# Optimization experiments

Measured on AMD Instinct MI355X. Metric: run time of the kernel, lower is better.

Reference implementation:

```python
import jax, jax.numpy as jnp
import numpy as np

B, C, T, H, W = 2, 512, 4, 32, 32
NH = 8          # num_heads
GROUPS = 32     # GroupNorm groups
EPS = 1e-5      # GroupNorm eps (torch default)


def setup_inputs() -> dict:
    key = jax.random.key(0)
    k0, k1, k2 = jax.random.split(key, 3)
    s = 0.02
    return {
        "x": jax.random.normal(k0, (B, C, T, H, W), jnp.float32),
        "gn_w": jnp.ones((C,), jnp.float32),
        "gn_b": jnp.zeros((C,), jnp.float32),
        "qkv_w": jax.random.normal(k1, (3 * C, C), jnp.float32) * s,
        "qkv_b": jnp.zeros((3 * C,), jnp.float32),
        "out_w": jax.random.normal(k2, (C, C), jnp.float32) * s,
        "out_b": jnp.zeros((C,), jnp.float32),
    }


def reference(x, gn_w, gn_b, qkv_w, qkv_b, out_w, out_b):
    Bb, Cc, Tt, Hh, Ww = x.shape
    N = Tt * Hh * Ww
    hd = Cc // NH

    # GroupNorm(32, C): normalize over (C//G, T, H, W) per group, biased var
    xg = x.reshape(Bb, GROUPS, -1)
    mean = jnp.mean(xg, axis=-1, keepdims=True)
    var = jnp.var(xg, axis=-1, keepdims=True)
    h = ((xg - mean) * jax.lax.rsqrt(var + EPS)).reshape(Bb, Cc, N)
    h = h * gn_w[None, :, None] + gn_b[None, :, None]

    # 1x1 Conv3d qkv == per-token linear over channels
    qkv = jnp.einsum('oc,bcn->bon', qkv_w, h) + qkv_b[None, :, None]
    qkv = qkv.reshape(Bb, 3, NH, hd, N).transpose(1, 0, 2, 4, 3)  # [3,B,nh,N,hd]
    q, k, v = qkv[0], qkv[1], qkv[2]

    scale = 1.0 / np.sqrt(hd).astype(np.float32)
    attn = jax.nn.softmax(jnp.einsum('bhnd,bhmd->bhnm', q, k) * scale, axis=-1)
    o = jnp.einsum('bhnm,bhmd->bhnd', attn, v)  # [B,nh,N,hd]

    # Faithful to original: h.permute(1,2,0,3).reshape(B,C,T,H,W)
    o = o.transpose(1, 2, 0, 3).reshape(Bb, Cc, N)
    o = jnp.einsum('oc,bcn->bon', out_w, o) + out_b[None, :, None]
    return x + o.reshape(Bb, Cc, Tt, Hh, Ww)
```

## Files before the change

### kernel.cpp

```cpp
#include <hip/hip_runtime.h>
#include <stdint.h>

#define B_    2
#define C_    512
#define NH_   8
#define HD_   64
#define N_    4096
#define G_    32
#define K_    512
#define EPS_  1e-5f
#define QSCALE_ 0.18033688011112042f

typedef __bf16 bf16;
typedef __attribute__((ext_vector_type(8))) __bf16 bf16x8;
typedef __attribute__((ext_vector_type(4))) float f32x4;

__global__ __launch_bounds__(256) void prep_k(const float* __restrict__ qkv_w,
                                              const float* __restrict__ out_w,
                                              const float* __restrict__ x,
                                              bf16* __restrict__ qkvwb,
                                              bf16* __restrict__ outwb,
                                              float* __restrict__ part) {
  const int blk = blockIdx.x;
  const int t = threadIdx.x;
  if (blk < 1024) {
    const int i = blk * 256 + t;
    const int n0 = (3 * C_ * C_) / 4;
    const float* s = (i < n0) ? qkv_w : out_w;
    bf16* d = (i < n0) ? qkvwb : outwb;
    const int k = (i < n0) ? i : i - n0;
    f32x4 v = *reinterpret_cast<const f32x4*>(s + (size_t)k * 4);
    bf16 o[4] = {(bf16)v[0], (bf16)v[1], (bf16)v[2], (bf16)v[3]};
    *reinterpret_cast<uint64_t*>(d + (size_t)k * 4) = *reinterpret_cast<uint64_t*>(o);
  } else {
    const int bb = blk - 1024;
    const float* p = x + (size_t)bb * 16384;
    float s1 = 0.f, s2 = 0.f;
    for (int i = 0; i < 16; ++i) {
      f32x4 v = *reinterpret_cast<const f32x4*>(p + (size_t)(i * 256 + t) * 4);
#pragma unroll
      for (int j = 0; j < 4; ++j) { float f = v[j]; s1 += f; s2 += f * f; }
    }
#pragma unroll
    for (int o = 32; o > 0; o >>= 1) { s1 += __shfl_down(s1, o); s2 += __shfl_down(s2, o); }
    __shared__ float a1[4], a2[4];
    if ((t & 63) == 0) { a1[t >> 6] = s1; a2[t >> 6] = s2; }
    __syncthreads();
    if (t == 0) {
      part[bb * 2]     = a1[0] + a1[1] + a1[2] + a1[3];
      part[bb * 2 + 1] = a2[0] + a2[1] + a2[2] + a2[3];
    }
  }
}

__global__ __launch_bounds__(256) void gn_apply_k(const float* __restrict__ x,
                                                  const float* __restrict__ part,
                                                  const float* __restrict__ gw,
                                                  const float* __restrict__ gb,
                                                  bf16* __restrict__ hT) {
  __shared__ float tile[64][65];
  const int n0 = blockIdx.x * 64, c0 = blockIdx.y * 64, b = blockIdx.z;
  const int t = threadIdx.x;
  {
    const int cc = t >> 2;
    const int nn = (t & 3) * 16;
    const int c = c0 + cc;
    const int bg = b * G_ + (c >> 4);
    float s1 = 0.f, s2 = 0.f;
#pragma unroll
    for (int q = 0; q < 4; ++q) {
      s1 += part[(bg * 4 + q) * 2];
      s2 += part[(bg * 4 + q) * 2 + 1];
    }
    const float mean = s1 * (1.f / 65536.f);
    const float var  = s2 * (1.f / 65536.f) - mean * mean;
    const float rstd = rsqrtf(var + EPS_);
    const float sw = gw[c] * rstd;
    const float sb = gb[c] - mean * sw;
    const float* xp = x + ((size_t)(b * C_ + c)) * N_ + n0 + nn;
#pragma unroll
    for (int q = 0; q < 4; ++q) {
      f32x4 v = *reinterpret_cast<const f32x4*>(xp + q * 4);
#pragma unroll
      for (int j = 0; j < 4; ++j) tile[cc][nn + q * 4 + j] = v[j] * sw + sb;
    }
  }
  __syncthreads();
  {
    const int rn = t >> 2;
    const int ch = (t & 3) * 16;
    bf16* hp = hT + ((size_t)b * N_ + n0 + rn) * C_ + c0 + ch;
    bf16x8 o0, o1;
#pragma unroll
    for (int j = 0; j < 8; ++j) {
      o0[j] = (bf16)tile[ch + j][rn];
      o1[j] = (bf16)tile[ch + 8 + j][rn];
    }
    *reinterpret_cast<bf16x8*>(hp)     = o0;
    *reinterpret_cast<bf16x8*>(hp + 8) = o1;
  }
}

template <int EPI>
__global__ __launch_bounds__(256) void gemm_bt_k(const bf16* __restrict__ A,
                                                 const bf16* __restrict__ BT,
                                                 const float* __restrict__ bias,
                                                 bf16* __restrict__ out0,
                                                 bf16* __restrict__ out1,
                                                 bf16* __restrict__ out2,
                                                 float* __restrict__ outf,
                                                 const float* __restrict__ xres) {
  __shared__ __align__(16) bf16 As[128][72];
  __shared__ __align__(16) bf16 Bs[128][72];
  const int t = threadIdx.x;
  const int w = t >> 6, lane = t & 63;
  const int quad = lane >> 4, l15 = lane & 15;
  const int m0 = blockIdx.y * 128, n0 = blockIdx.x * 128, b = blockIdx.z;
  const bf16* Ab = A + (size_t)m0 * K_;
  const bf16* Bb = BT + ((size_t)b * N_ + n0) * K_;
  const int srow = t >> 1;
  const int sk = (t & 1) * 32;

  f32x4 acc[4][4] = {};

  for (int kc = 0; kc < K_ / 64; ++kc) {
    __syncthreads();
    {
      const bf16* ag = Ab + (size_t)srow * K_ + kc * 64 + sk;
      const bf16* bg = Bb + (size_t)srow * K_ + kc * 64 + sk;
#pragma unroll
      for (int c = 0; c < 4; ++c) {
        *reinterpret_cast<bf16x8*>(&As[srow][sk + c * 8]) = *reinterpret_cast<const bf16x8*>(ag + c * 8);
        *reinterpret_cast<bf16x8*>(&Bs[srow][sk + c * 8]) = *reinterpret_cast<const bf16x8*>(bg + c * 8);
      }
    }
    __syncthreads();
    bf16x8 af[4][2], bfv[4][2];
#pragma unroll
    for (int i = 0; i < 4; ++i) {
      af[i][0] = *reinterpret_cast<const bf16x8*>(&As[(w >> 1) * 64 + i * 16 + l15][quad * 8]);
      af[i][1] = *reinterpret_cast<const bf16x8*>(&As[(w >> 1) * 64 + i * 16 + l15][quad * 8 + 32]);
    }
#pragma unroll
    for (int j = 0; j < 4; ++j) {
      bfv[j][0] = *reinterpret_cast<const bf16x8*>(&Bs[(w & 1) * 64 + j * 16 + l15][quad * 8]);
      bfv[j][1] = *reinterpret_cast<const bf16x8*>(&Bs[(w & 1) * 64 + j * 16 + l15][quad * 8 + 32]);
    }
#pragma unroll
    for (int i = 0; i < 4; ++i)
#pragma unroll
      for (int j = 0; j < 4; ++j) {
        acc[i][j] = __builtin_amdgcn_mfma_f32_16x16x32_bf16(af[i][0], bfv[j][0], acc[i][j], 0, 0, 0);
        acc[i][j] = __builtin_amdgcn_mfma_f32_16x16x32_bf16(af[i][1], bfv[j][1], acc[i][j], 0, 0, 0);
      }
  }

  const int rowbase = m0 + (w >> 1) * 64;
  const int colbase = n0 + (w & 1) * 64;
  if (EPI == 0) {
    const int which = m0 >> 9;
    if (which < 2) {
      bf16* dst = (which == 0) ? out0 : out1;
      const float sc = (which == 0) ? (float)QSCALE_ : 1.0f;
#pragma unroll
      for (int i = 0; i < 4; ++i) {
        const int mbase = rowbase + i * 16 + quad * 4;
        const int head = (mbase >> 6) & 7, d0 = mbase & 63;
        float bi[4];
#pragma unroll
        for (int r = 0; r < 4; ++r) bi[r] = bias[mbase + r];
#pragma unroll
        for (int j = 0; j < 4; ++j) {
          const int n = colbase + j * 16 + l15;
          union { bf16 h[4]; uint64_t u; } pk;
#pragma unroll
          for (int r = 0; r < 4; ++r) pk.h[r] = (bf16)((acc[i][j][r] + bi[r]) * sc);
          *reinterpret_cast<uint64_t*>(dst + ((size_t)(b * NH_ + head) * N_ + n) * HD_ + d0) = pk.u;
        }
      }
    } else {
#pragma unroll
      for (int i = 0; i < 4; ++i) {
        const int mbase = rowbase + i * 16 + quad * 4;
        const int head = (mbase >> 6) & 7;
#pragma unroll
        for (int r = 0; r < 4; ++r) {
          const int d = (mbase + r) & 63;
          const float bi = bias[mbase + r];
#pragma unroll
          for (int j = 0; j < 4; ++j) {
            const int n = colbase + j * 16 + l15;
            out2[((size_t)(b * NH_ + head) * HD_ + d) * N_ + n] = (bf16)(acc[i][j][r] + bi);
          }
        }
      }
    }
  } else {
#pragma unroll
    for (int i = 0; i < 4; ++i) {
#pragma unroll
      for (int r = 0; r < 4; ++r) {
        const int m = rowbase + i * 16 + quad * 4 + r;
        const float bi = bias[m];
#pragma unroll
        for (int j = 0; j < 4; ++j) {
          const int n = colbase + j * 16 + l15;
          const size_t idx = ((size_t)(b * C_ + m)) * N_ + n;
          outf[idx] = acc[i][j][r] + bi + xres[idx];
        }
      }
    }
  }
}

__global__ __launch_bounds__(256, 3) void attn_k(const bf16* __restrict__ qb,
                                                 const bf16* __restrict__ kb,
                                                 const bf16* __restrict__ vb,
                                                 bf16* __restrict__ oT) {
  __shared__ __align__(16) char smem[46080];
  bf16* Ps = (bf16*)(smem + 36864);
  bf16* Ot = (bf16*)smem;

  const int t = threadIdx.x;
  const int w = t >> 6, lane = t & 63, quad = lane >> 4, l15 = lane & 15;
  const int rblk = blockIdx.x;
  const int bh = blockIdx.y, head = bh & 7, b = bh >> 3;
  const bf16* qh = qb + (size_t)bh * N_ * HD_;
  const bf16* kh = kb + (size_t)bh * N_ * HD_;
  const bf16* vh = vb + (size_t)bh * HD_ * N_;

  bf16x8 qa[2][2];
#pragma unroll
  for (int b2 = 0; b2 < 2; ++b2) {
    const int bd = w + 4 * b2;
    const bf16* qp = qh + ((size_t)((bd * 16 + l15) * 32 + rblk)) * HD_ + quad * 8;
    qa[b2][0] = *reinterpret_cast<const bf16x8*>(qp);
    qa[b2][1] = *reinterpret_cast<const bf16x8*>(qp + 32);
  }

  f32x4 acc[2][4] = {};
  float lsum[2][4] = {};

  const int sr = t >> 3, sc = (t & 7) * 8;
  const int s0 = (sr & 3) * 16 + (sr >> 2);
  const int s1 = ((sr + 32) & 3) * 16 + ((sr + 32) >> 2);
  bf16* Pw = Ps + w * 1152;

  {
    *reinterpret_cast<bf16x8*>((bf16*)smem + s0 * 72 + sc) =
        *reinterpret_cast<const bf16x8*>(kh + (size_t)sr * HD_ + sc);
    *reinterpret_cast<bf16x8*>((bf16*)smem + s1 * 72 + sc) =
        *reinterpret_cast<const bf16x8*>(kh + (size_t)(sr + 32) * HD_ + sc);
    bf16* Vb0 = (bf16*)(smem + 9216);
    *reinterpret_cast<bf16x8*>(Vb0 + sr * 72 + sc) =
        *reinterpret_cast<const bf16x8*>(vh + (size_t)sr * N_ + sc);
    *reinterpret_cast<bf16x8*>(Vb0 + (sr + 32) * 72 + sc) =
        *reinterpret_cast<const bf16x8*>(vh + (size_t)(sr + 32) * N_ + sc);
  }
  __syncthreads();

  for (int kt = 0; kt < 64; ++kt) {
    bf16* curK = (bf16*)(smem + (kt & 1) * 18432);
    bf16* curV = (bf16*)(smem + (kt & 1) * 18432 + 9216);

    bf16x8 kr0, kr1, vr0, vr1;
    if (kt != 63) {
      const bf16* kg = kh + ((size_t)(kt + 1) * 64) * HD_;
      kr0 = *reinterpret_cast<const bf16x8*>(kg + (size_t)sr * HD_ + sc);
      kr1 = *reinterpret_cast<const bf16x8*>(kg + (size_t)(sr + 32) * HD_ + sc);
      const bf16* vg = vh + (size_t)(kt + 1) * 64;
      vr0 = *reinterpret_cast<const bf16x8*>(vg + (size_t)sr * N_ + sc);
      vr1 = *reinterpret_cast<const bf16x8*>(vg + (size_t)(sr + 32) * N_ + sc);
    }

    bf16x8 kf0[4], kf1[4];
#pragma unroll
    for (int mt = 0; mt < 4; ++mt) {
      kf0[mt] = *reinterpret_cast<const bf16x8*>(curK + (mt * 16 + l15) * 72 + quad * 8);
      kf1[mt] = *reinterpret_cast<const bf16x8*>(curK + (mt * 16 + l15) * 72 + quad * 8 + 32);
    }
    f32x4 S[2][4];
#pragma unroll
    for (int b2 = 0; b2 < 2; ++b2)
#pragma unroll
      for (int mt = 0; mt < 4; ++mt) {
        f32x4 zz = {0.f, 0.f, 0.f, 0.f};
        zz = __builtin_amdgcn_mfma_f32_16x16x32_bf16(qa[b2][0], kf0[mt], zz, 0, 0, 0);
        S[b2][mt] = __builtin_amdgcn_mfma_f32_16x16x32_bf16(qa[b2][1], kf1[mt], zz, 0, 0, 0);
      }

    bf16x8 vf0[4], vf1[4];
#pragma unroll
    for (int dt = 0; dt < 4; ++dt) {
      vf0[dt] = *reinterpret_cast<const bf16x8*>(curV + (dt * 16 + l15) * 72 + quad * 8);
      vf1[dt] = *reinterpret_cast<const bf16x8*>(curV + (dt * 16 + l15) * 72 + quad * 8 + 32);
    }

#pragma unroll
    for (int b2 = 0; b2 < 2; ++b2) {
#pragma unroll
      for (int r = 0; r < 4; ++r) {
        float p0 = __builtin_amdgcn_exp2f(S[b2][0][r]);
        float p1 = __builtin_amdgcn_exp2f(S[b2][1][r]);
        float p2 = __builtin_amdgcn_exp2f(S[b2][2][r]);
        float p3 = __builtin_amdgcn_exp2f(S[b2][3][r]);
        lsum[b2][r] += (p0 + p1) + (p2 + p3);
        union { bf16 h[4]; uint64_t u; } pk;
        pk.h[0] = (bf16)p0; pk.h[1] = (bf16)p1; pk.h[2] = (bf16)p2; pk.h[3] = (bf16)p3;
        *reinterpret_cast<uint64_t*>(Pw + (quad * 4 + r) * 72 + l15 * 4) = pk.u;
      }
      asm volatile("s_waitcnt lgkmcnt(0)" ::: "memory");
      bf16x8 pa0 = *reinterpret_cast<const bf16x8*>(Pw + l15 * 72 + quad * 8);
      bf16x8 pa1 = *reinterpret_cast<const bf16x8*>(Pw + l15 * 72 + quad * 8 + 32);
#pragma unroll
      for (int dt = 0; dt < 4; ++dt) {
        acc[b2][dt] = __builtin_amdgcn_mfma_f32_16x16x32_bf16(pa0, vf0[dt], acc[b2][dt], 0, 0, 0);
        acc[b2][dt] = __builtin_amdgcn_mfma_f32_16x16x32_bf16(pa1, vf1[dt], acc[b2][dt], 0, 0, 0);
      }
    }

    if (kt != 63) {
      bf16* nK = (bf16*)(smem + ((kt + 1) & 1) * 18432);
      bf16* nV = (bf16*)(smem + ((kt + 1) & 1) * 18432 + 9216);
      *reinterpret_cast<bf16x8*>(nK + s0 * 72 + sc) = kr0;
      *reinterpret_cast<bf16x8*>(nK + s1 * 72 + sc) = kr1;
      *reinterpret_cast<bf16x8*>(nV + sr * 72 + sc) = vr0;
      *reinterpret_cast<bf16x8*>(nV + (sr + 32) * 72 + sc) = vr1;
    }
    __syncthreads();
  }

  float inv[2][4];
#pragma unroll
  for (int b2 = 0; b2 < 2; ++b2)
#pragma unroll
    for (int r = 0; r < 4; ++r) {
      float l = lsum[b2][r];
#pragma unroll
      for (int o = 1; o < 16; o <<= 1) l += __shfl_xor(l, o);
      inv[b2][r] = 1.f / l;
    }

#pragma unroll
  for (int b2 = 0; b2 < 2; ++b2) {
    const int bd = w + 4 * b2;
#pragma unroll
    for (int dt = 0; dt < 4; ++dt) {
      union { bf16 h[4]; uint64_t u; } o4;
#pragma unroll
      for (int r = 0; r < 4; ++r) o4.h[r] = (bf16)(acc[b2][dt][r] * inv[b2][r]);
      *reinterpret_cast<uint64_t*>(Ot + (dt * 16 + l15) * 136 + bd * 16 + quad * 4) = o4.u;
    }
  }
  __syncthreads();
  {
    const int d = t >> 2, ic = (t & 3) * 32;
    bf16* op = oT + (size_t)(head >> 2) * N_ * C_ +
               ((size_t)(rblk * 128 + b * 64 + d)) * C_ + (head & 3) * 128 + ic;
#pragma unroll
    for (int c = 0; c < 4; ++c)
      *reinterpret_cast<bf16x8*>(op + c * 8) =
          *reinterpret_cast<const bf16x8*>(Ot + d * 136 + ic + c * 8);
  }
}

extern "C" void kernel_launch(void* const* d_in, const int* in_sizes, int n_in,
                              void* d_out, int out_size, void* d_ws, size_t ws_size,
                              hipStream_t stream) {
  const float* x     = (const float*)d_in[0];
  const float* gn_w  = (const float*)d_in[1];
  const float* gn_b  = (const float*)d_in[2];
  const float* qkv_w = (const float*)d_in[3];
  const float* qkv_b = (const float*)d_in[4];
  const float* out_w = (const float*)d_in[5];
  const float* out_b = (const float*)d_in[6];
  float* out = (float*)d_out;

  char* ws = (char*)d_ws;
  const size_t SZ = (size_t)B_ * C_ * N_ * sizeof(bf16);
  float* part  = (float*)ws;
  bf16* hT    = (bf16*)(ws + 4096);
  bf16* qbuf  = (bf16*)(ws + 4096 + SZ);
  bf16* kbuf  = (bf16*)(ws + 4096 + 2 * SZ);
  bf16* vbuf  = (bf16*)(ws + 4096 + 3 * SZ);
  bf16* oT    = (bf16*)(ws + 4096 + 4 * SZ);
  bf16* qkvwb = (bf16*)(ws + 4096 + 5 * SZ);
  bf16* outwb = qkvwb + (size_t)3 * C_ * C_;

  prep_k<<<dim3(1280), dim3(256), 0, stream>>>(qkv_w, out_w, x, qkvwb, outwb, part);
  gn_apply_k<<<dim3(N_ / 64, C_ / 64, B_), dim3(256), 0, stream>>>(x, part, gn_w, gn_b, hT);
  gemm_bt_k<0><<<dim3(N_ / 128, (3 * C_) / 128, B_), dim3(256), 0, stream>>>(
      qkvwb, hT, qkv_b, qbuf, kbuf, vbuf, nullptr, nullptr);
  attn_k<<<dim3(32, B_ * NH_), dim3(256), 0, stream>>>(qbuf, kbuf, vbuf, oT);
  gemm_bt_k<1><<<dim3(N_ / 128, C_ / 128, B_), dim3(256), 0, stream>>>(
      outwb, oT, out_b, nullptr, nullptr, nullptr, out, x);
}
```

Measured before the change: 215.6 us.

## Split attention over key halves and combine partial outputs in separate kernel

Attention blocks now process half of the keys each (grid z=2), writing unnormalized bf16 partial outputs and per-row softmax sums. A new combine kernel adds the two partials and divides by the summed denominators. This doubles the number of attention blocks to fill more CUs, at the cost of extra memory traffic, an extra launch, and bf16 rounding of partial sums.

```diff
diff --git a/kernel.cpp b/kernel.cpp
--- a/kernel.cpp
+++ b/kernel.cpp
@@ -216,7 +216,9 @@
 __global__ __launch_bounds__(256, 3) void attn_k(const bf16* __restrict__ qb,
                                                  const bf16* __restrict__ kb,
                                                  const bf16* __restrict__ vb,
-                                                 bf16* __restrict__ oT) {
+                                                 bf16* __restrict__ po0,
+                                                 bf16* __restrict__ po1,
+                                                 float* __restrict__ pl) {
   __shared__ __align__(16) char smem[46080];
   bf16* Ps = (bf16*)(smem + 36864);
   bf16* Ot = (bf16*)smem;
@@ -225,9 +227,10 @@
   const int w = t >> 6, lane = t & 63, quad = lane >> 4, l15 = lane & 15;
   const int rblk = blockIdx.x;
   const int bh = blockIdx.y, head = bh & 7, b = bh >> 3;
+  const int z = blockIdx.z;
   const bf16* qh = qb + (size_t)bh * N_ * HD_;
-  const bf16* kh = kb + (size_t)bh * N_ * HD_;
-  const bf16* vh = vb + (size_t)bh * HD_ * N_;
+  const bf16* kh = kb + (size_t)bh * N_ * HD_ + (size_t)z * 2048 * HD_;
+  const bf16* vh = vb + (size_t)bh * HD_ * N_ + (size_t)z * 2048;
 
   bf16x8 qa[2][2];
 #pragma unroll
@@ -259,12 +262,12 @@
   }
   __syncthreads();
 
-  for (int kt = 0; kt < 64; ++kt) {
+  for (int kt = 0; kt < 32; ++kt) {
     bf16* curK = (bf16*)(smem + (kt & 1) * 18432);
     bf16* curV = (bf16*)(smem + (kt & 1) * 18432 + 9216);
 
     bf16x8 kr0, kr1, vr0, vr1;
-    if (kt != 63) {
+    if (kt != 31) {
       const bf16* kg = kh + ((size_t)(kt + 1) * 64) * HD_;
       kr0 = *reinterpret_cast<const bf16x8*>(kg + (size_t)sr * HD_ + sc);
       kr1 = *reinterpret_cast<const bf16x8*>(kg + (size_t)(sr + 32) * HD_ + sc);
@@ -319,7 +322,7 @@
       }
     }
 
-    if (kt != 63) {
+    if (kt != 31) {
       bf16* nK = (bf16*)(smem + ((kt + 1) & 1) * 18432);
       bf16* nV = (bf16*)(smem + ((kt + 1) & 1) * 18432 + 9216);
       *reinterpret_cast<bf16x8*>(nK + s0 * 72 + sc) = kr0;
@@ -330,16 +333,19 @@
     __syncthreads();
   }
 
-  float inv[2][4];
-#pragma unroll
-  for (int b2 = 0; b2 < 2; ++b2)
+  bf16* po = (z == 0) ? po0 : po1;
+#pragma unroll
+  for (int b2 = 0; b2 < 2; ++b2) {
+    const int bd = w + 4 * b2;
 #pragma unroll
     for (int r = 0; r < 4; ++r) {
       float l = lsum[b2][r];
 #pragma unroll
       for (int o = 1; o < 16; o <<= 1) l += __shfl_xor(l, o);
-      inv[b2][r] = 1.f / l;
-    }
+      if (l15 == 0)
+        pl[((size_t)z * 16 + bh) * N_ + (bd * 16 + quad * 4 + r) * 32 + rblk] = l;
+    }
+  }
 
 #pragma unroll
   for (int b2 = 0; b2 < 2; ++b2) {
@@ -348,20 +354,48 @@
     for (int dt = 0; dt < 4; ++dt) {
       union { bf16 h[4]; uint64_t u; } o4;
 #pragma unroll
-      for (int r = 0; r < 4; ++r) o4.h[r] = (bf16)(acc[b2][dt][r] * inv[b2][r]);
+      for (int r = 0; r < 4; ++r) o4.h[r] = (bf16)acc[b2][dt][r];
       *reinterpret_cast<uint64_t*>(Ot + (dt * 16 + l15) * 136 + bd * 16 + quad * 4) = o4.u;
     }
   }
   __syncthreads();
   {
     const int d = t >> 2, ic = (t & 3) * 32;
-    bf16* op = oT + (size_t)(head >> 2) * N_ * C_ +
+    bf16* op = po + (size_t)(head >> 2) * N_ * C_ +
                ((size_t)(rblk * 128 + b * 64 + d)) * C_ + (head & 3) * 128 + ic;
 #pragma unroll
     for (int c = 0; c < 4; ++c)
       *reinterpret_cast<bf16x8*>(op + c * 8) =
           *reinterpret_cast<const bf16x8*>(Ot + d * 136 + ic + c * 8);
   }
+}
+
+__global__ __launch_bounds__(256) void comb_k(const bf16* __restrict__ a0,
+                                              const bf16* __restrict__ a1,
+                                              const float* __restrict__ pl,
+                                              bf16* __restrict__ oT) {
+  const int tid = blockIdx.x * 256 + threadIdx.x;
+  const int e8 = tid * 8;
+  const int cp = e8 & 511;
+  const int np = (e8 >> 9) & 4095;
+  const int bp = e8 >> 21;
+  const int head = (bp << 2) | (cp >> 7);
+  const int rblk = np >> 7;
+  const int b = (np >> 6) & 1;
+  const int bh = b * NH_ + head;
+  const int ibase = cp & 127;
+  const float* l0 = pl + (size_t)bh * N_ + rblk;
+  const float* l1 = l0 + (size_t)16 * N_;
+  bf16x8 x0 = *reinterpret_cast<const bf16x8*>(a0 + e8);
+  bf16x8 x1 = *reinterpret_cast<const bf16x8*>(a1 + e8);
+  bf16x8 o;
+#pragma unroll
+  for (int j = 0; j < 8; ++j) {
+    const int off = (ibase + j) * 32;
+    const float l = l0[off] + l1[off];
+    o[j] = (bf16)(((float)x0[j] + (float)x1[j]) * __builtin_amdgcn_rcpf(l));
+  }
+  *reinterpret_cast<bf16x8*>(oT + e8) = o;
 }
 
 extern "C" void kernel_launch(void* const* d_in, const int* in_sizes, int n_in,
@@ -386,12 +420,15 @@
   bf16* oT    = (bf16*)(ws + 4096 + 4 * SZ);
   bf16* qkvwb = (bf16*)(ws + 4096 + 5 * SZ);
   bf16* outwb = qkvwb + (size_t)3 * C_ * C_;
+  bf16* po1   = outwb + (size_t)C_ * C_;
+  float* pL   = (float*)(po1 + (size_t)B_ * C_ * N_);
 
   prep_k<<<dim3(1280), dim3(256), 0, stream>>>(qkv_w, out_w, x, qkvwb, outwb, part);
   gn_apply_k<<<dim3(N_ / 64, C_ / 64, B_), dim3(256), 0, stream>>>(x, part, gn_w, gn_b, hT);
   gemm_bt_k<0><<<dim3(N_ / 128, (3 * C_) / 128, B_), dim3(256), 0, stream>>>(
       qkvwb, hT, qkv_b, qbuf, kbuf, vbuf, nullptr, nullptr);
-  attn_k<<<dim3(32, B_ * NH_), dim3(256), 0, stream>>>(qbuf, kbuf, vbuf, oT);
+  attn_k<<<dim3(32, B_ * NH_, 2), dim3(256), 0, stream>>>(qbuf, kbuf, vbuf, hT, po1, pL);
+  comb_k<<<dim3((B_ * C_ * N_) / 2048), dim3(256), 0, stream>>>(hT, po1, pL, oT);
   gemm_bt_k<1><<<dim3(N_ / 128, C_ / 128, B_), dim3(256), 0, stream>>>(
       outwb, oT, out_b, nullptr, nullptr, nullptr, out, x);
 }
```

New measurement: 245.8 us. 14.0% more time.

## Keep softmax probabilities in registers via transposed MFMA operand order

Applied to the files above, without the earlier changes.

Swaps the MFMA operand order so the score tile comes out transposed (keys along rows), letting exp'd probabilities be packed straight into the B-operand registers for the PV MFMA. This removes the per-wave LDS round trip (store, waitcnt, reload) for P and its shared buffer, and reorders the K staging rows to match. The row-sum reduction shrinks to two cross-quad shuffles, but the epilogue now gathers the output transpose with scalar LDS reads. The launch-bounds occupancy hint drops from 3 to 2 waves-per-SIMD blocks.

```diff
diff --git a/kernel.cpp b/kernel.cpp
--- a/kernel.cpp
+++ b/kernel.cpp
@@ -213,12 +213,11 @@
   }
 }
 
-__global__ __launch_bounds__(256, 3) void attn_k(const bf16* __restrict__ qb,
+__global__ __launch_bounds__(256, 2) void attn_k(const bf16* __restrict__ qb,
                                                  const bf16* __restrict__ kb,
                                                  const bf16* __restrict__ vb,
                                                  bf16* __restrict__ oT) {
-  __shared__ __align__(16) char smem[46080];
-  bf16* Ps = (bf16*)(smem + 36864);
+  __shared__ __align__(16) char smem[36864];
   bf16* Ot = (bf16*)smem;
 
   const int t = threadIdx.x;
@@ -239,12 +238,11 @@
   }
 
   f32x4 acc[2][4] = {};
-  float lsum[2][4] = {};
+  float lsum[2] = {0.f, 0.f};
 
   const int sr = t >> 3, sc = (t & 7) * 8;
-  const int s0 = (sr & 3) * 16 + (sr >> 2);
-  const int s1 = ((sr + 32) & 3) * 16 + ((sr + 32) >> 2);
-  bf16* Pw = Ps + w * 1152;
+  const int s0 = ((sr >> 2) & 1) * 16 + ((sr >> 3) & 3) * 4 + (sr & 3);
+  const int s1 = s0 + 32;
 
   {
     *reinterpret_cast<bf16x8*>((bf16*)smem + s0 * 72 + sc) =
@@ -285,8 +283,8 @@
 #pragma unroll
       for (int mt = 0; mt < 4; ++mt) {
         f32x4 zz = {0.f, 0.f, 0.f, 0.f};
-        zz = __builtin_amdgcn_mfma_f32_16x16x32_bf16(qa[b2][0], kf0[mt], zz, 0, 0, 0);
-        S[b2][mt] = __builtin_amdgcn_mfma_f32_16x16x32_bf16(qa[b2][1], kf1[mt], zz, 0, 0, 0);
+        zz = __builtin_amdgcn_mfma_f32_16x16x32_bf16(kf0[mt], qa[b2][0], zz, 0, 0, 0);
+        S[b2][mt] = __builtin_amdgcn_mfma_f32_16x16x32_bf16(kf1[mt], qa[b2][1], zz, 0, 0, 0);
       }
 
     bf16x8 vf0[4], vf1[4];
@@ -298,24 +296,23 @@
 
 #pragma unroll
     for (int b2 = 0; b2 < 2; ++b2) {
+      union { bf16 h[8]; bf16x8 v; } f0, f1;
+      float s = 0.f;
 #pragma unroll
       for (int r = 0; r < 4; ++r) {
         float p0 = __builtin_amdgcn_exp2f(S[b2][0][r]);
         float p1 = __builtin_amdgcn_exp2f(S[b2][1][r]);
         float p2 = __builtin_amdgcn_exp2f(S[b2][2][r]);
         float p3 = __builtin_amdgcn_exp2f(S[b2][3][r]);
-        lsum[b2][r] += (p0 + p1) + (p2 + p3);
-        union { bf16 h[4]; uint64_t u; } pk;
-        pk.h[0] = (bf16)p0; pk.h[1] = (bf16)p1; pk.h[2] = (bf16)p2; pk.h[3] = (bf16)p3;
-        *reinterpret_cast<uint64_t*>(Pw + (quad * 4 + r) * 72 + l15 * 4) = pk.u;
-      }
-      asm volatile("s_waitcnt lgkmcnt(0)" ::: "memory");
-      bf16x8 pa0 = *reinterpret_cast<const bf16x8*>(Pw + l15 * 72 + quad * 8);
-      bf16x8 pa1 = *reinterpret_cast<const bf16x8*>(Pw + l15 * 72 + quad * 8 + 32);
+        s += (p0 + p1) + (p2 + p3);
+        f0.h[r] = (bf16)p0; f0.h[4 + r] = (bf16)p1;
+        f1.h[r] = (bf16)p2; f1.h[4 + r] = (bf16)p3;
+      }
+      lsum[b2] += s;
 #pragma unroll
       for (int dt = 0; dt < 4; ++dt) {
-        acc[b2][dt] = __builtin_amdgcn_mfma_f32_16x16x32_bf16(pa0, vf0[dt], acc[b2][dt], 0, 0, 0);
-        acc[b2][dt] = __builtin_amdgcn_mfma_f32_16x16x32_bf16(pa1, vf1[dt], acc[b2][dt], 0, 0, 0);
+        acc[b2][dt] = __builtin_amdgcn_mfma_f32_16x16x32_bf16(vf0[dt], f0.v, acc[b2][dt], 0, 0, 0);
+        acc[b2][dt] = __builtin_amdgcn_mfma_f32_16x16x32_bf16(vf1[dt], f1.v, acc[b2][dt], 0, 0, 0);
       }
     }
 
@@ -330,26 +327,24 @@
     __syncthreads();
   }
 
-  float inv[2][4];
-#pragma unroll
-  for (int b2 = 0; b2 < 2; ++b2)
-#pragma unroll
-    for (int r = 0; r < 4; ++r) {
-      float l = lsum[b2][r];
-#pragma unroll
-      for (int o = 1; o < 16; o <<= 1) l += __shfl_xor(l, o);
-      inv[b2][r] = 1.f / l;
-    }
-
+  float inv[2];
 #pragma unroll
   for (int b2 = 0; b2 < 2; ++b2) {
-    const int bd = w + 4 * b2;
+    float l = lsum[b2];
+    l += __shfl_xor(l, 16);
+    l += __shfl_xor(l, 32);
+    inv[b2] = 1.f / l;
+  }
+
+#pragma unroll
+  for (int b2 = 0; b2 < 2; ++b2) {
+    const int i = (w + 4 * b2) * 16 + l15;
 #pragma unroll
     for (int dt = 0; dt < 4; ++dt) {
       union { bf16 h[4]; uint64_t u; } o4;
 #pragma unroll
-      for (int r = 0; r < 4; ++r) o4.h[r] = (bf16)(acc[b2][dt][r] * inv[b2][r]);
-      *reinterpret_cast<uint64_t*>(Ot + (dt * 16 + l15) * 136 + bd * 16 + quad * 4) = o4.u;
+      for (int r = 0; r < 4; ++r) o4.h[r] = (bf16)(acc[b2][dt][r] * inv[b2]);
+      *reinterpret_cast<uint64_t*>(Ot + i * 72 + dt * 16 + quad * 4) = o4.u;
     }
   }
   __syncthreads();
@@ -358,9 +353,12 @@
     bf16* op = oT + (size_t)(head >> 2) * N_ * C_ +
                ((size_t)(rblk * 128 + b * 64 + d)) * C_ + (head & 3) * 128 + ic;
 #pragma unroll
-    for (int c = 0; c < 4; ++c)
-      *reinterpret_cast<bf16x8*>(op + c * 8) =
-          *reinterpret_cast<const bf16x8*>(Ot + d * 136 + ic + c * 8);
+    for (int c = 0; c < 4; ++c) {
+      union { bf16 h[8]; bf16x8 v; } o8;
+#pragma unroll
+      for (int j = 0; j < 8; ++j) o8.h[j] = Ot[(ic + c * 8 + j) * 72 + d];
+      *reinterpret_cast<bf16x8*>(op + c * 8) = o8.v;
+    }
   }
 }
 
```

Result: faster. 203.8 us (-5.5%).
